# Kernel tuning notes

Hardware: AMD Instinct MI355X
Metric: run time of the kernel (lower is better)

Reference implementation:

```python
import jax, jax.numpy as jnp
import numpy as np

# ---- config (mirrors cfg / init kwargs) ----
FEAT_STRIDE = 16
IM_DIMS = (1024, 1024)          # (height, width)
ANCHOR_SCALES = (8, 16, 32)
ANCHOR_RATIOS = (0.5, 1.0, 2.0)
PRE_NMS_TOPN = 6000             # eval mode (cfg_key=1)
POST_NMS_TOPN = 300
NMS_THRESH = 0.7
MIN_SIZE = 16


def _generate_base_anchors(base_size=16, ratios=ANCHOR_RATIOS, scales=ANCHOR_SCALES):
    """py-faster-rcnn generate_anchors, in numpy (static)."""
    def mk(ws, hs, xc, yc):
        return np.stack([xc - 0.5 * (ws - 1), yc - 0.5 * (hs - 1),
                         xc + 0.5 * (ws - 1), yc + 0.5 * (hs - 1)], axis=1)
    base = np.array([0, 0, base_size - 1, base_size - 1], dtype=np.float64)
    w = base[2] - base[0] + 1; h = base[3] - base[1] + 1
    xc = base[0] + 0.5 * (w - 1); yc = base[1] + 0.5 * (h - 1)
    # ratio enum
    size = w * h
    ws = np.round(np.sqrt(size / np.array(ratios)))
    hs = np.round(ws * np.array(ratios))
    ratio_anchors = mk(ws, hs, xc, yc)
    # scale enum
    out = []
    for a in ratio_anchors:
        aw = a[2] - a[0] + 1; ah = a[3] - a[1] + 1
        axc = a[0] + 0.5 * (aw - 1); ayc = a[1] + 0.5 * (ah - 1)
        out.append(mk(aw * np.array(scales), ah * np.array(scales), axc, ayc))
    return np.concatenate(out, axis=0).astype(np.float32)  # [A,4]


def _all_anchors(H, W):
    base = _generate_base_anchors()                       # [A,4]
    sx = np.arange(W) * FEAT_STRIDE
    sy = np.arange(H) * FEAT_STRIDE
    sx, sy = np.meshgrid(sx, sy)
    shifts = np.stack([sx.ravel(), sy.ravel(), sx.ravel(), sy.ravel()], axis=1)  # [H*W,4]
    anchors = shifts[:, None, :].astype(np.float32) + base[None, :, :]
    return anchors.reshape(-1, 4)                         # [H*W*A, 4]


def setup_inputs() -> dict:
    key = jax.random.key(0)
    k1, k2 = jax.random.split(key)
    H, W, A = 64, 64, 9
    rpn_cls_score = jax.random.normal(k1, (1, H, W, 2 * A), dtype=jnp.float32)
    rpn_bbox_pred = jax.random.normal(k2, (1, H, W, 4 * A), dtype=jnp.float32)
    return {"rpn_cls_score": rpn_cls_score, "rpn_bbox_pred": rpn_bbox_pred}


def _proposals(rpn_cls_score, rpn_bbox_pred):
    _, H, W, C2 = rpn_cls_score.shape
    A = C2 // 2
    # rpn_softmax: per-anchor 2-way softmax, foreground prob
    scores = jax.nn.softmax(rpn_cls_score.reshape(H, W, A, 2), axis=-1)[..., 1].reshape(-1)  # [N]
    deltas = rpn_bbox_pred.reshape(-1, 4)                  # [N,4]
    anchors = jnp.asarray(_all_anchors(H, W))              # [N,4]
    # bbox_transform_inv
    aw = anchors[:, 2] - anchors[:, 0] + 1.0
    ah = anchors[:, 3] - anchors[:, 1] + 1.0
    axc = anchors[:, 0] + 0.5 * aw
    ayc = anchors[:, 1] + 0.5 * ah
    dx, dy, dw, dh = deltas[:, 0], deltas[:, 1], deltas[:, 2], deltas[:, 3]
    pxc = dx * aw + axc; pyc = dy * ah + ayc
    pw = jnp.exp(dw) * aw; ph = jnp.exp(dh) * ah
    x1 = pxc - 0.5 * pw; y1 = pyc - 0.5 * ph
    x2 = pxc + 0.5 * pw; y2 = pyc + 0.5 * ph
    # clip to image
    im_h, im_w = IM_DIMS
    x1 = jnp.clip(x1, 0.0, im_w - 1.0); x2 = jnp.clip(x2, 0.0, im_w - 1.0)
    y1 = jnp.clip(y1, 0.0, im_h - 1.0); y2 = jnp.clip(y2, 0.0, im_h - 1.0)
    boxes = jnp.stack([x1, y1, x2, y2], axis=1)            # [N,4]
    # filter too-small boxes by masking their score
    valid = ((x2 - x1 + 1.0) >= MIN_SIZE) & ((y2 - y1 + 1.0) >= MIN_SIZE)
    scores = jnp.where(valid, scores, -jnp.inf)
    return boxes, scores


def _nms_keep(boxes, K):
    """Greedy NMS keep-mask over score-descending boxes [K,4]."""
    x1, y1, x2, y2 = boxes[:, 0], boxes[:, 1], boxes[:, 2], boxes[:, 3]
    areas = (x2 - x1 + 1.0) * (y2 - y1 + 1.0)
    ix1 = jnp.maximum(x1[:, None], x1[None, :])
    iy1 = jnp.maximum(y1[:, None], y1[None, :])
    ix2 = jnp.minimum(x2[:, None], x2[None, :])
    iy2 = jnp.minimum(y2[:, None], y2[None, :])
    iw = jnp.maximum(ix2 - ix1 + 1.0, 0.0)
    ih = jnp.maximum(iy2 - iy1 + 1.0, 0.0)
    inter = iw * ih
    iou = inter / (areas[:, None] + areas[None, :] - inter)  # [K,K]
    idxs = jnp.arange(K)
    def body(i, keep):
        sup = keep[i] & (iou[i] > NMS_THRESH) & (idxs > i)
        return keep & ~sup
    return jax.lax.fori_loop(0, K, body, jnp.ones((K,), bool))


def reference(rpn_cls_score, rpn_bbox_pred):
    boxes, scores = _proposals(rpn_cls_score, rpn_bbox_pred)
    K = min(PRE_NMS_TOPN, scores.shape[0])
    top_scores, order = jax.lax.top_k(scores, K)           # score-descending
    top_boxes = boxes[order]                               # [K,4]
    keep = _nms_keep(top_boxes, K)
    sel_scores = jnp.where(keep, top_scores, -jnp.inf)
    _, idx = jax.lax.top_k(sel_scores, POST_NMS_TOPN)      # kept, in score order
    out_boxes = top_boxes[idx]                             # [post,4]
    blob = jnp.concatenate([jnp.zeros((POST_NMS_TOPN, 1), out_boxes.dtype), out_boxes], axis=1)
    return blob                                            # [post,5] (batch_idx, x1,y1,x2,y2)
```

## Files before the change

### kernel.cpp

```cpp
#include <hip/hip_runtime.h>
#include <stdint.h>

typedef unsigned long long u64;
typedef unsigned int u32;

#define N_ANCH 36864
#define WGRID 64
#define A_PER 9
#define KTOP 6000
#define NOUT 300
#define NBIN 8192
#define NCHK 94
#define INF_BIN 0

__constant__ float c_ax1[9] = {-84.f,-176.f,-360.f,-56.f,-120.f,-248.f,-36.f,-80.f,-168.f};
__constant__ float c_ay1[9] = {-40.f,-88.f,-184.f,-56.f,-120.f,-248.f,-80.f,-168.f,-344.f};
__constant__ float c_aw[9]  = {184.f,368.f,736.f,128.f,256.f,512.f,88.f,176.f,352.f};
__constant__ float c_ah[9]  = {96.f,192.f,384.f,128.f,256.f,512.f,176.f,352.f,704.f};

__device__ __forceinline__ u32 binof(u32 u) {
    if (u < 0x80000000u) return 0u;
    if (u < 0xBF000000u) return 1u + ((u - 0x80000000u) >> 22);
    return 256u + ((u - 0xBF000000u) >> 11);
}

__global__ __launch_bounds__(1024) void proposal_kernel(const float* __restrict__ cls,
                                                        const float* __restrict__ dlt,
                                                        u64* __restrict__ keys,
                                                        float4* __restrict__ boxes,
                                                        u32* __restrict__ hist) {
    __shared__ u32 lh[NBIN];
    const int t = threadIdx.x;
    for (int b = t; b < NBIN; b += 1024) lh[b] = 0;
    __syncthreads();

    int i = blockIdx.x * 1024 + t;
    int a  = i % A_PER;
    int hw = i / A_PER;
    int wx = hw % WGRID;
    int hy = hw / WGRID;

    float l0 = cls[hw * 18 + 2 * a];
    float l1 = cls[hw * 18 + 2 * a + 1];
    float m  = fmaxf(l0, l1);
    float e0 = expf(l0 - m), e1 = expf(l1 - m);
    float s  = e1 / (e0 + e1);

    const float* d = dlt + hw * 36 + 4 * a;
    float dx = d[0], dy = d[1], dw = d[2], dh = d[3];
    float aw = c_aw[a], ah = c_ah[a];
    float axc = (c_ax1[a] + 16.f * (float)wx) + 0.5f * aw;
    float ayc = (c_ay1[a] + 16.f * (float)hy) + 0.5f * ah;

    float pxc = dx * aw + axc;
    float pyc = dy * ah + ayc;
    float pw  = expf(dw) * aw;
    float ph  = expf(dh) * ah;
    float x1 = pxc - 0.5f * pw, y1 = pyc - 0.5f * ph;
    float x2 = pxc + 0.5f * pw, y2 = pyc + 0.5f * ph;
    x1 = fminf(fmaxf(x1, 0.f), 1023.f);
    x2 = fminf(fmaxf(x2, 0.f), 1023.f);
    y1 = fminf(fmaxf(y1, 0.f), 1023.f);
    y2 = fminf(fmaxf(y2, 0.f), 1023.f);
    bool valid = ((x2 - x1 + 1.f) >= 16.f) && ((y2 - y1 + 1.f) >= 16.f);
    float sc = valid ? s : -__builtin_huge_valf();

    u32 sb  = __float_as_uint(sc);
    u32 ord = (sb & 0x80000000u) ? ~sb : (sb | 0x80000000u);
    u64 key = ((u64)ord << 32) | (u32)(~(u32)i);
    keys[i]  = key;
    boxes[i] = make_float4(x1, y1, x2, y2);

    u64 infb = __ballot(!valid);
    if (valid) {
        atomicAdd(&lh[binof(ord)], 1u);
    } else {
        int lane = t & 63;
        if (lane == __builtin_ctzll(infb))
            atomicAdd(&lh[INF_BIN], (u32)__popcll(infb));
    }
    __syncthreads();
    for (int b = t; b < NBIN; b += 1024) {
        u32 v = lh[b];
        if (v) atomicAdd(&hist[b], v);
    }
}

__global__ __launch_bounds__(1024) void scan_kernel(const u32* __restrict__ hist,
                                                    u32* __restrict__ binStart,
                                                    u32* __restrict__ gEV) {
    __shared__ u32 sh[1024];
    int t = threadIdx.x;
    if (t == 0) gEV[1] = KTOP;
    int hi = NBIN - 1 - 8 * t;
    u32 cnt[8];
    u32 sum = 0;
#pragma unroll
    for (int k = 0; k < 8; ++k) { cnt[k] = hist[hi - k]; sum += cnt[k]; }
    sh[t] = sum;
    __syncthreads();
    for (int d = 1; d < 1024; d <<= 1) {
        u32 v = (t >= d) ? sh[t - d] : 0;
        __syncthreads();
        sh[t] += v;
        __syncthreads();
    }
    u32 run = sh[t] - sum;
#pragma unroll
    for (int k = 0; k < 8; ++k) {
        int b = hi - k;
        binStart[b] = run;
        u32 end = run + cnt[k];
        if (run < KTOP && end >= KTOP) gEV[0] = end;
        run = end;
    }
}

__global__ void scatter_kernel(const u64* __restrict__ keys,
                               const u32* __restrict__ binStart,
                               u32* __restrict__ cursor,
                               u64* __restrict__ scat) {
    int i = blockIdx.x * blockDim.x + threadIdx.x;
    if (i >= N_ANCH) return;
    u64 k = keys[i];
    u32 b = binof((u32)(k >> 32));
    u32 s = binStart[b];
    if (s < KTOP) {
        u32 p = s + atomicAdd(&cursor[b], 1u);
        scat[p] = k;
    }
}

__global__ void rank_kernel(const u64* __restrict__ scat,
                            const u32* __restrict__ binStart,
                            const u32* __restrict__ hist,
                            const float4* __restrict__ boxes,
                            const u32* __restrict__ gEV,
                            float4* __restrict__ topBoxes,
                            int* __restrict__ gV) {
    int i = blockIdx.x * blockDim.x + threadIdx.x;
    u32 E = gEV[0];
    if (i >= (int)E) return;
    u64 k = scat[i];
    u32 b = binof((u32)(k >> 32));
    u32 s = binStart[b], c = hist[b];
    u32 r = s;
    for (u32 j = s; j < s + c; ++j) r += (scat[j] > k) ? 1u : 0u;
    if (r < KTOP) {
        int idx = (int)(~(u32)k);
        topBoxes[r] = boxes[idx];
        if (!(k >> 63)) atomicMin(gV, (int)r);
    }
}

__device__ __forceinline__ bool iou_gt(float4 a, float areaA, float4 b, float areaB) {
    float ix1 = fmaxf(a.x, b.x), iy1 = fmaxf(a.y, b.y);
    float ix2 = fminf(a.z, b.z), iy2 = fminf(a.w, b.w);
    float iw = fmaxf(ix2 - ix1 + 1.0f, 0.0f);
    float ih = fmaxf(iy2 - iy1 + 1.0f, 0.0f);
    float inter = iw * ih;
    float iou = inter / (areaA + areaB - inter);
    return iou > 0.7f;
}

__global__ __launch_bounds__(1024) void nms_out_kernel(const float4* __restrict__ topBoxes,
                                                       const u32* __restrict__ gEV,
                                                       float* __restrict__ out) {
    __shared__ float4 cbox[2][64];
    __shared__ float  ca[2][64];
    __shared__ u64    intra[2][64];
    __shared__ u64    supw[16];
    __shared__ u64    keepw[NCHK];
    __shared__ float4 kbox[NOUT];
    __shared__ float  karea[NOUT];
    __shared__ u32    scanbuf[1024];
    __shared__ int    s_nkept;

    const int t = threadIdx.x;
    const int lane = t & 63;
    const int w = t >> 6;
    if (t < NCHK) keepw[t] = 0;
    if (t == 0) s_nkept = 0;
    const int V = (int)gEV[1];
    const int nchunks = (V + 63) >> 6;

    if (t < 64) {
        float4 b = make_float4(0.f, 0.f, 0.f, 0.f);
        if (t < V) b = topBoxes[t];
        cbox[0][t] = b;
        ca[0][t]   = (b.z - b.x + 1.f) * (b.w - b.y + 1.f);
        intra[0][t] = 0;
    }
    __syncthreads();

    for (int c = 0; c < nchunks; ++c) {
        const int p = c & 1;
        const int base = c * 64;
        const int csz = min(64, V - base);
        const int nk = s_nkept;
        bool sup = false;
        if (lane < csz) {
            float4 bb = cbox[p][lane]; float ab = ca[p][lane];
            for (int k = w; k < nk; k += 16) {
                if (iou_gt(bb, ab, kbox[k], karea[k])) { sup = true; break; }
            }
        }
        u64 bal = __ballot(sup);
        if (lane == 0) supw[w] = bal;
        if (lane < csz) {
            float4 bb = cbox[p][lane]; float ab = ca[p][lane];
            u64 m = 0;
            int j0 = lane + 1;
            j0 += ((w - j0) % 16 + 16) % 16;
            for (int j = j0; j < csz; j += 16)
                if (iou_gt(bb, ab, cbox[p][j], ca[p][j])) m |= (1ULL << j);
            if (m) atomicOr(&intra[p][lane], m);
        }
        __syncthreads();
        if (w == 0) {
            u64 row = intra[p][lane];
            u64 sup64 = 0;
#pragma unroll
            for (int q = 0; q < 16; ++q) sup64 |= supw[q];
            u64 alive = ~sup64;
            if (csz < 64) alive &= ((1ULL << csz) - 1ULL);
            u64 cand = alive, kb = 0;
            const int nk_base = s_nkept;
            int nk2 = nk_base;
            while (cand && nk2 < NOUT) {
                int b = __builtin_ctzll(cand);
                cand &= cand - 1;
                kb |= (1ULL << b);
                ++nk2;
                cand &= ~__shfl(row, b, 64);
            }
            if ((kb >> lane) & 1ULL) {
                int pos = nk_base + __popcll(kb & ((1ULL << lane) - 1ULL));
                kbox[pos]  = cbox[p][lane];
                karea[pos] = ca[p][lane];
            }
            if (lane == 0) { keepw[c] = kb; s_nkept = nk2; }
        } else if (w == 1) {
            int nb = base + 64 + lane;
            float4 b = make_float4(0.f, 0.f, 0.f, 0.f);
            if (nb < V) b = topBoxes[nb];
            cbox[p ^ 1][lane] = b;
            ca[p ^ 1][lane]   = (b.z - b.x + 1.f) * (b.w - b.y + 1.f);
            intra[p ^ 1][lane] = 0;
        }
        __syncthreads();
        if (s_nkept >= NOUT) break;
    }

    const int n1 = s_nkept;
    for (int r = t; r < n1; r += 1024) {
        float4 b = kbox[r];
        out[r * 5 + 0] = 0.f;
        out[r * 5 + 1] = b.x; out[r * 5 + 2] = b.y;
        out[r * 5 + 3] = b.z; out[r * 5 + 4] = b.w;
    }
    if (n1 < NOUT) {
        __syncthreads();
        const int per = 6;
        int r0 = t * per, r1 = min(r0 + per, KTOP);
        u32 cnt = 0;
        for (int r = r0; r < r1; ++r)
            cnt += ((keepw[r >> 6] >> (r & 63)) & 1ULL) ? 0u : 1u;
        scanbuf[t] = cnt;
        __syncthreads();
        for (int d = 1; d < 1024; d <<= 1) {
            u32 v = (t >= d) ? scanbuf[t - d] : 0;
            __syncthreads();
            scanbuf[t] += v;
            __syncthreads();
        }
        int ord = n1 + (int)(scanbuf[t] - cnt);
        for (int r = r0; r < r1 && ord < NOUT; ++r) {
            if (!((keepw[r >> 6] >> (r & 63)) & 1ULL)) {
                float4 b = topBoxes[r];
                out[ord * 5 + 0] = 0.f;
                out[ord * 5 + 1] = b.x; out[ord * 5 + 2] = b.y;
                out[ord * 5 + 3] = b.z; out[ord * 5 + 4] = b.w;
                ++ord;
            }
        }
    }
}

extern "C" void kernel_launch(void* const* d_in, const int* in_sizes, int n_in,
                              void* d_out, int out_size, void* d_ws, size_t ws_size,
                              hipStream_t stream) {
    const float* cls = (const float*)d_in[0];
    const float* dlt = (const float*)d_in[1];
    float* out = (float*)d_out;
    char* ws = (char*)d_ws;
    u64*    keys     = (u64*)   (ws);
    u64*    scat     = (u64*)   (ws + 294912);
    float4* boxes    = (float4*)(ws + 589824);
    float4* topBoxes = (float4*)(ws + 1179648);
    u32*    hist     = (u32*)   (ws + 1275648);
    u32*    cursor   = (u32*)   (ws + 1308416);
    u32*    binStart = (u32*)   (ws + 1341184);
    u32*    gEV      = (u32*)   (ws + 1373952);

    hipMemsetAsync(hist, 0, 2 * NBIN * sizeof(u32), stream);
    proposal_kernel<<<36, 1024, 0, stream>>>(cls, dlt, keys, boxes, hist);
    scan_kernel<<<1, 1024, 0, stream>>>(hist, binStart, gEV);
    scatter_kernel<<<(N_ANCH + 255) / 256, 256, 0, stream>>>(keys, binStart, cursor, scat);
    rank_kernel<<<(N_ANCH + 255) / 256, 256, 0, stream>>>(scat, binStart, hist, boxes, gEV,
                                                          topBoxes, (int*)&gEV[1]);
    nms_out_kernel<<<1, 1024, 0, stream>>>(topBoxes, gEV, out);
}
```

Measured before the change: 118.9 us.

## Precompute NMS IoU bitmasks in a parallel kernel and reduce with single wave

Adds a multi-block mask kernel that computes the upper-triangular IoU suppression bitmask over the top-sorted boxes. It also writes diagonal and next-diagonal blocks separately, so the serial NMS pass becomes a single-wave bitwise walk that ORs in precomputed rows. This is meant to remove the per-chunk block-wide syncs and IoU work from the single-block serial loop. The cost is that IoU is computed for every candidate pair even when 300 boxes are kept early, plus a multi-MB mask write and one extra launch. It also shrinks the histogram bin count and vectorizes the logit and delta loads.

```diff
diff --git a/kernel.cpp b/kernel.cpp
--- a/kernel.cpp
+++ b/kernel.cpp
@@ -9,9 +9,10 @@
 #define A_PER 9
 #define KTOP 6000
 #define NOUT 300
-#define NBIN 8192
+#define NBIN 5120
 #define NCHK 94
 #define INF_BIN 0
+#define PCAP 8
 
 __constant__ float c_ax1[9] = {-84.f,-176.f,-360.f,-56.f,-120.f,-248.f,-36.f,-80.f,-168.f};
 __constant__ float c_ay1[9] = {-40.f,-88.f,-184.f,-56.f,-120.f,-248.f,-80.f,-168.f,-344.f};
@@ -40,14 +41,14 @@
     int wx = hw % WGRID;
     int hy = hw / WGRID;
 
-    float l0 = cls[hw * 18 + 2 * a];
-    float l1 = cls[hw * 18 + 2 * a + 1];
+    float2 lp = *(const float2*)(cls + hw * 18 + 2 * a);
+    float l0 = lp.x, l1 = lp.y;
     float m  = fmaxf(l0, l1);
     float e0 = expf(l0 - m), e1 = expf(l1 - m);
     float s  = e1 / (e0 + e1);
 
-    const float* d = dlt + hw * 36 + 4 * a;
-    float dx = d[0], dy = d[1], dw = d[2], dh = d[3];
+    float4 dd = *(const float4*)(dlt + hw * 36 + 4 * a);
+    float dx = dd.x, dy = dd.y, dw = dd.z, dh = dd.w;
     float aw = c_aw[a], ah = c_ah[a];
     float axc = (c_ax1[a] + 16.f * (float)wx) + 0.5f * aw;
     float ayc = (c_ay1[a] + 16.f * (float)hy) + 0.5f * ah;
@@ -92,11 +93,11 @@
     __shared__ u32 sh[1024];
     int t = threadIdx.x;
     if (t == 0) gEV[1] = KTOP;
-    int hi = NBIN - 1 - 8 * t;
-    u32 cnt[8];
+    int hi = NBIN - 1 - 5 * t;
+    u32 cnt[5];
     u32 sum = 0;
 #pragma unroll
-    for (int k = 0; k < 8; ++k) { cnt[k] = hist[hi - k]; sum += cnt[k]; }
+    for (int k = 0; k < 5; ++k) { cnt[k] = hist[hi - k]; sum += cnt[k]; }
     sh[t] = sum;
     __syncthreads();
     for (int d = 1; d < 1024; d <<= 1) {
@@ -107,7 +108,7 @@
     }
     u32 run = sh[t] - sum;
 #pragma unroll
-    for (int k = 0; k < 8; ++k) {
+    for (int k = 0; k < 5; ++k) {
         int b = hi - k;
         binStart[b] = run;
         u32 end = run + cnt[k];
@@ -163,127 +164,152 @@
     return iou > 0.7f;
 }
 
+__global__ __launch_bounds__(256) void mask_kernel(const float4* __restrict__ topBoxes,
+                                                   const u32* __restrict__ gEV,
+                                                   u64* __restrict__ M,
+                                                   u64* __restrict__ D0,
+                                                   u64* __restrict__ D1) {
+    const int V = (int)gEV[1];
+    const int nch = (V + 63) >> 6;
+    const int cw = blockIdx.x;
+    const int r0 = blockIdx.y * 4;
+    if (cw >= nch || r0 > cw || r0 >= nch) return;
+    __shared__ float4 cb[64];
+    __shared__ float ca[64];
+    const int t = threadIdx.x;
+    const int lane = t & 63;
+    if (t < 64) {
+        int cj = cw * 64 + t;
+        float4 b = (cj < V) ? topBoxes[cj] : make_float4(0.f, 0.f, -8.f, -8.f);
+        cb[t] = b;
+        ca[t] = (b.z - b.x + 1.f) * (b.w - b.y + 1.f);
+    }
+    __syncthreads();
+    const int r = r0 + (t >> 6);
+    if (r > cw || r >= nch) return;
+    const int i = r * 64 + lane;
+    if (i >= V) return;
+    float4 bi = topBoxes[i];
+    float ai = (bi.z - bi.x + 1.f) * (bi.w - bi.y + 1.f);
+    u64 m = 0;
+#pragma unroll 4
+    for (int j = 0; j < 64; ++j)
+        if (iou_gt(bi, ai, cb[j], ca[j])) m |= (1ULL << j);
+    if (cw == r) { m &= ~((2ULL << lane) - 1ULL); D0[i] = m; }
+    if (cw == r + 1) D1[i] = m;
+    M[(u64)i * NCHK + cw] = m;
+}
+
 __global__ __launch_bounds__(1024) void nms_out_kernel(const float4* __restrict__ topBoxes,
                                                        const u32* __restrict__ gEV,
+                                                       const u64* __restrict__ M,
+                                                       const u64* __restrict__ D0,
+                                                       const u64* __restrict__ D1,
                                                        float* __restrict__ out) {
-    __shared__ float4 cbox[2][64];
-    __shared__ float  ca[2][64];
-    __shared__ u64    intra[2][64];
-    __shared__ u64    supw[16];
-    __shared__ u64    keepw[NCHK];
-    __shared__ float4 kbox[NOUT];
-    __shared__ float  karea[NOUT];
-    __shared__ u32    scanbuf[1024];
-    __shared__ int    s_nkept;
-
+    __shared__ u64 keepw[NCHK];
+    __shared__ u32 scanbuf[1024];
     const int t = threadIdx.x;
     const int lane = t & 63;
-    const int w = t >> 6;
     if (t < NCHK) keepw[t] = 0;
-    if (t == 0) s_nkept = 0;
     const int V = (int)gEV[1];
-    const int nchunks = (V + 63) >> 6;
+    const int nch = (V + 63) >> 6;
+    __syncthreads();
 
     if (t < 64) {
-        float4 b = make_float4(0.f, 0.f, 0.f, 0.f);
-        if (t < V) b = topBoxes[t];
-        cbox[0][t] = b;
-        ca[0][t]   = (b.z - b.x + 1.f) * (b.w - b.y + 1.f);
-        intra[0][t] = 0;
-    }
-    __syncthreads();
-
-    for (int c = 0; c < nchunks; ++c) {
-        const int p = c & 1;
-        const int base = c * 64;
-        const int csz = min(64, V - base);
-        const int nk = s_nkept;
-        bool sup = false;
-        if (lane < csz) {
-            float4 bb = cbox[p][lane]; float ab = ca[p][lane];
-            for (int k = w; k < nk; k += 16) {
-                if (iou_gt(bb, ab, kbox[k], karea[k])) { sup = true; break; }
+        u64 remA = 0, remB = 0, carry = 0;
+        u64 pendA[PCAP], pendB[PCAP];
+#pragma unroll
+        for (int k = 0; k < PCAP; ++k) { pendA[k] = 0; pendB[k] = 0; }
+        int np = 0;
+        u64 d0 = 0, d1 = 0;
+        if (lane < V) {
+            d0 = D0[lane];
+            if (nch > 1) d1 = D1[lane];
+        }
+        int nkept = 0;
+        for (int c = 0; c < nch; ++c) {
+            u64 rw = ((c < 64) ? __shfl(remA, c) : __shfl(remB, c - 64)) | carry;
+            int rem_n = V - c * 64;
+            u64 aliveM = (rem_n >= 64) ? ~0ULL : ((1ULL << rem_n) - 1ULL);
+            u64 cand = ~rw & aliveM;
+            u64 nd0 = 0, nd1 = 0;
+            if (c + 1 < nch) {
+                int idx = (c + 1) * 64 + lane;
+                if (idx < V) {
+                    nd0 = D0[idx];
+                    if (c + 2 < nch) nd1 = D1[idx];
+                }
             }
+            u64 kb = 0, ncarry = 0;
+            while (cand) {
+                int b = __builtin_ctzll(cand);
+                kb |= (1ULL << b);
+                cand &= ~((1ULL << b) | __shfl(d0, b));
+                ncarry |= __shfl(d1, b);
+            }
+            if (lane == 0) keepw[c] = kb;
+            nkept += __popcll(kb);
+#pragma unroll
+            for (int k = 0; k < PCAP; ++k)
+                if (k < np) { remA |= pendA[k]; remB |= pendB[k]; }
+            u64 kk = kb;
+            int nn = 0;
+#pragma unroll
+            for (int k = 0; k < PCAP; ++k) {
+                if (kk) {
+                    int b = __builtin_ctzll(kk);
+                    kk &= kk - 1;
+                    const u64* row = M + (u64)(c * 64 + b) * NCHK;
+                    pendA[k] = row[lane];
+                    pendB[k] = (lane + 64 < NCHK) ? row[lane + 64] : 0;
+                    ++nn;
+                }
+            }
+            np = nn;
+            while (kk) {
+                int b = __builtin_ctzll(kk);
+                kk &= kk - 1;
+                const u64* row = M + (u64)(c * 64 + b) * NCHK;
+                remA |= row[lane];
+                if (lane + 64 < NCHK) remB |= row[lane + 64];
+            }
+            carry = ncarry;
+            d0 = nd0;
+            d1 = nd1;
+            if (nkept >= NOUT) break;
         }
-        u64 bal = __ballot(sup);
-        if (lane == 0) supw[w] = bal;
-        if (lane < csz) {
-            float4 bb = cbox[p][lane]; float ab = ca[p][lane];
-            u64 m = 0;
-            int j0 = lane + 1;
-            j0 += ((w - j0) % 16 + 16) % 16;
-            for (int j = j0; j < csz; j += 16)
-                if (iou_gt(bb, ab, cbox[p][j], ca[p][j])) m |= (1ULL << j);
-            if (m) atomicOr(&intra[p][lane], m);
+    }
+    __syncthreads();
+
+    const int per = 6;
+    int r0 = t * per;
+    int r1 = min(r0 + per, KTOP);
+    u32 cnt = 0;
+    for (int r = r0; r < r1; ++r)
+        cnt += (u32)((keepw[r >> 6] >> (r & 63)) & 1ULL);
+    scanbuf[t] = cnt;
+    __syncthreads();
+    for (int d = 1; d < 1024; d <<= 1) {
+        u32 v = (t >= d) ? scanbuf[t - d] : 0;
+        __syncthreads();
+        scanbuf[t] += v;
+        __syncthreads();
+    }
+    const int total = (int)scanbuf[1023];
+    const int n1 = min(total, NOUT);
+    int kp = (int)(scanbuf[t] - cnt);
+    for (int r = r0; r < r1; ++r) {
+        int kept = (int)((keepw[r >> 6] >> (r & 63)) & 1ULL);
+        int pos = kept ? kp : (n1 + r - kp);
+        if (pos < NOUT) {
+            float4 b = topBoxes[r];
+            out[pos * 5 + 0] = 0.f;
+            out[pos * 5 + 1] = b.x;
+            out[pos * 5 + 2] = b.y;
+            out[pos * 5 + 3] = b.z;
+            out[pos * 5 + 4] = b.w;
         }
-        __syncthreads();
-        if (w == 0) {
-            u64 row = intra[p][lane];
-            u64 sup64 = 0;
-#pragma unroll
-            for (int q = 0; q < 16; ++q) sup64 |= supw[q];
-            u64 alive = ~sup64;
-            if (csz < 64) alive &= ((1ULL << csz) - 1ULL);
-            u64 cand = alive, kb = 0;
-            const int nk_base = s_nkept;
-            int nk2 = nk_base;
-            while (cand && nk2 < NOUT) {
-                int b = __builtin_ctzll(cand);
-                cand &= cand - 1;
-                kb |= (1ULL << b);
-                ++nk2;
-                cand &= ~__shfl(row, b, 64);
-            }
-            if ((kb >> lane) & 1ULL) {
-                int pos = nk_base + __popcll(kb & ((1ULL << lane) - 1ULL));
-                kbox[pos]  = cbox[p][lane];
-                karea[pos] = ca[p][lane];
-            }
-            if (lane == 0) { keepw[c] = kb; s_nkept = nk2; }
-        } else if (w == 1) {
-            int nb = base + 64 + lane;
-            float4 b = make_float4(0.f, 0.f, 0.f, 0.f);
-            if (nb < V) b = topBoxes[nb];
-            cbox[p ^ 1][lane] = b;
-            ca[p ^ 1][lane]   = (b.z - b.x + 1.f) * (b.w - b.y + 1.f);
-            intra[p ^ 1][lane] = 0;
-        }
-        __syncthreads();
-        if (s_nkept >= NOUT) break;
-    }
-
-    const int n1 = s_nkept;
-    for (int r = t; r < n1; r += 1024) {
-        float4 b = kbox[r];
-        out[r * 5 + 0] = 0.f;
-        out[r * 5 + 1] = b.x; out[r * 5 + 2] = b.y;
-        out[r * 5 + 3] = b.z; out[r * 5 + 4] = b.w;
-    }
-    if (n1 < NOUT) {
-        __syncthreads();
-        const int per = 6;
-        int r0 = t * per, r1 = min(r0 + per, KTOP);
-        u32 cnt = 0;
-        for (int r = r0; r < r1; ++r)
-            cnt += ((keepw[r >> 6] >> (r & 63)) & 1ULL) ? 0u : 1u;
-        scanbuf[t] = cnt;
-        __syncthreads();
-        for (int d = 1; d < 1024; d <<= 1) {
-            u32 v = (t >= d) ? scanbuf[t - d] : 0;
-            __syncthreads();
-            scanbuf[t] += v;
-            __syncthreads();
-        }
-        int ord = n1 + (int)(scanbuf[t] - cnt);
-        for (int r = r0; r < r1 && ord < NOUT; ++r) {
-            if (!((keepw[r >> 6] >> (r & 63)) & 1ULL)) {
-                float4 b = topBoxes[r];
-                out[ord * 5 + 0] = 0.f;
-                out[ord * 5 + 1] = b.x; out[ord * 5 + 2] = b.y;
-                out[ord * 5 + 3] = b.z; out[ord * 5 + 4] = b.w;
-                ++ord;
-            }
-        }
+        kp += kept;
     }
 }
 
@@ -299,9 +325,12 @@
     float4* boxes    = (float4*)(ws + 589824);
     float4* topBoxes = (float4*)(ws + 1179648);
     u32*    hist     = (u32*)   (ws + 1275648);
-    u32*    cursor   = (u32*)   (ws + 1308416);
-    u32*    binStart = (u32*)   (ws + 1341184);
-    u32*    gEV      = (u32*)   (ws + 1373952);
+    u32*    cursor   = (u32*)   (ws + 1296128);
+    u32*    binStart = (u32*)   (ws + 1316608);
+    u32*    gEV      = (u32*)   (ws + 1337088);
+    u64*    D0       = (u64*)   (ws + 1337344);
+    u64*    D1       = (u64*)   (ws + 1385344);
+    u64*    M        = (u64*)   (ws + 1433344);
 
     hipMemsetAsync(hist, 0, 2 * NBIN * sizeof(u32), stream);
     proposal_kernel<<<36, 1024, 0, stream>>>(cls, dlt, keys, boxes, hist);
@@ -309,5 +338,6 @@
     scatter_kernel<<<(N_ANCH + 255) / 256, 256, 0, stream>>>(keys, binStart, cursor, scat);
     rank_kernel<<<(N_ANCH + 255) / 256, 256, 0, stream>>>(scat, binStart, hist, boxes, gEV,
                                                           topBoxes, (int*)&gEV[1]);
-    nms_out_kernel<<<1, 1024, 0, stream>>>(topBoxes, gEV, out);
-}
+    mask_kernel<<<dim3(NCHK, (NCHK + 3) / 4), 256, 0, stream>>>(topBoxes, gEV, M, D0, D1);
+    nms_out_kernel<<<1, 1024, 0, stream>>>(topBoxes, gEV, M, D0, D1, out);
+}
```

After: 221.4 us. 86.2% more time.
